# Kernel tuning notes

Measured on AMD Instinct MI355X. Metric: run time of the kernel, lower is better.

## Reference

```python
import math
import jax, jax.numpy as jnp
import numpy as np

N, T, D, H = 256, 128, 1024, 1024


def setup_inputs() -> dict:
    key = jax.random.key(0)
    k1, k2, k3, k4, k5 = jax.random.split(key, 5)
    x = jax.random.normal(k1, (N, T, D), dtype=jnp.float32)
    A = jax.random.normal(k2, (N, H, 4, 4), dtype=jnp.float32)
    Wx = jax.random.normal(k3, (D, 4 * H), dtype=jnp.float32) / math.sqrt(D)
    Wh = jax.random.normal(k4, (H, 4 * H), dtype=jnp.float32) / math.sqrt(H)
    Wattn = jax.random.normal(k5, (H, 4 * H), dtype=jnp.float32) / math.sqrt(H)
    b = jnp.zeros((4 * H,), dtype=jnp.float32)
    return {"x": x, "A": A, "Wx": Wx, "Wh": Wh, "Wattn": Wattn, "b": b}


def reference(x, A, Wx, Wh, Wattn, b):
    n, h = A.shape[0], A.shape[1]
    Af = A.reshape(n, h, 16)           # (N, H, 16) flattened 4x4 feature map
    h0 = Af.mean(axis=2)               # mean-pooled global feature inits h0, c0
    scale = 1.0 / math.sqrt(h)

    def step(carry, x_t):
        prev_h, prev_c = carry
        # scaled dot-product attention over 16 spatial locations
        logits = jnp.einsum("nh,nhl->nl", prev_h, Af) * scale   # (N, 16)
        w = jax.nn.softmax(logits, axis=1)
        attn = jnp.einsum("nhl,nl->nh", Af, w)                  # (N, H)
        # LSTM gates
        pre = x_t @ Wx + prev_h @ Wh + attn @ Wattn + b          # (N, 4H)
        i, f, o, g = jnp.split(pre, 4, axis=1)
        next_c = jax.nn.sigmoid(f) * prev_c + jax.nn.sigmoid(i) * jnp.tanh(g)
        next_h = jax.nn.sigmoid(o) * jnp.tanh(next_c)
        return (next_h, next_c), next_h

    xs = jnp.swapaxes(x, 0, 1)         # (T, N, D)
    _, hs = jax.lax.scan(step, (h0, h0), xs)
    return jnp.swapaxes(hs, 0, 1)      # (N, T, H)
```

## Files before the change

kernel.cpp:

```cpp
#include <hip/hip_runtime.h>
#include <hip/hip_bf16.h>

#define NB 256
#define TT 128
#define DD 1024
#define HH 1024
#define FH 4096
#define KTOT 3072

typedef __attribute__((ext_vector_type(4))) float f32x4;
typedef __attribute__((ext_vector_type(8))) short short8;

__device__ __forceinline__ unsigned short f2bf(float f) {
    union { float f; unsigned u; } v; v.f = f;
    unsigned u = v.u;
    u += 0x7FFFu + ((u >> 16) & 1u);
    return (unsigned short)(u >> 16);
}
__device__ __forceinline__ float bf2f(unsigned short u) {
    union { unsigned u; float f; } v; v.u = ((unsigned)u) << 16; return v.f;
}
__device__ __forceinline__ float sigm(float v) { return 1.f / (1.f + __expf(-v)); }
__device__ __forceinline__ float tanhf_(float v) { return 1.f - 2.f / (__expf(2.f * v) + 1.f); }

__device__ __forceinline__ void bmap(int bid, int& m0, int& j0) {
    int xx = bid & 7, yy = (bid >> 3) & 7, mt = bid >> 6;
    m0 = mt * 64;
    j0 = (xx * 8 + yy) * 16;
}

__device__ __forceinline__ short8 pack8(float4 v0, float4 v1) {
    short8 r;
    r[0] = (short)f2bf(v0.x); r[1] = (short)f2bf(v0.y);
    r[2] = (short)f2bf(v0.z); r[3] = (short)f2bf(v0.w);
    r[4] = (short)f2bf(v1.x); r[5] = (short)f2bf(v1.y);
    r[6] = (short)f2bf(v1.z); r[7] = (short)f2bf(v1.w);
    return r;
}

__global__ __launch_bounds__(256) void wt_prep(const float* __restrict__ Wx,
                                               const float* __restrict__ Wh,
                                               const float* __restrict__ Wattn,
                                               unsigned short* __restrict__ Wt) {
    __shared__ unsigned short tile[64][65];
    int k0 = blockIdx.x * 64;
    int c0 = blockIdx.y * 64;
    const float* src; int kl0;
    if (k0 < 1024)      { src = Wx;    kl0 = k0; }
    else if (k0 < 2048) { src = Wh;    kl0 = k0 - 1024; }
    else                { src = Wattn; kl0 = k0 - 2048; }
    int tid = threadIdx.x;
    int r = tid >> 2;
    int ch = (tid & 3) << 4;
    const float* p = src + (size_t)(kl0 + r) * FH + c0 + ch;
#pragma unroll
    for (int i = 0; i < 16; i += 4) {
        float4 v = *reinterpret_cast<const float4*>(p + i);
        tile[r][ch + i + 0] = f2bf(v.x);
        tile[r][ch + i + 1] = f2bf(v.y);
        tile[r][ch + i + 2] = f2bf(v.z);
        tile[r][ch + i + 3] = f2bf(v.w);
    }
    __syncthreads();
    alignas(16) unsigned short vals[16];
#pragma unroll
    for (int i = 0; i < 16; ++i) vals[i] = tile[ch + i][r];
    unsigned short* q = Wt + (size_t)(c0 + r) * KTOT + k0 + ch;
    *reinterpret_cast<uint4*>(q)     = *reinterpret_cast<uint4*>(&vals[0]);
    *reinterpret_cast<uint4*>(q + 8) = *reinterpret_cast<uint4*>(&vals[8]);
}

__global__ __launch_bounds__(256) void zero_buf(float* __restrict__ p, int n) {
    int i = blockIdx.x * 256 + threadIdx.x;
    if (i < n) p[i] = 0.f;
}

__global__ __launch_bounds__(256) void xconv(const float* __restrict__ x,
                                             unsigned short* __restrict__ xbf) {
    size_t i = ((size_t)blockIdx.x * 256 + threadIdx.x) * 8;
    float4 v0 = *reinterpret_cast<const float4*>(x + i);
    float4 v1 = *reinterpret_cast<const float4*>(x + i + 4);
    short8 p = pack8(v0, v1);
    *reinterpret_cast<short8*>(xbf + i) = p;
}

__global__ __launch_bounds__(256) void afT_prep(const float* __restrict__ A,
                                                unsigned short* __restrict__ AfT) {
    int n = blockIdx.x;
#pragma unroll
    for (int pass = 0; pass < 4; ++pass) {
        int hh = pass * 256 + threadIdx.x;
        const float4* p = reinterpret_cast<const float4*>(A + ((size_t)n * HH + hh) * 16);
        float4 a0 = p[0], a1 = p[1], a2 = p[2], a3 = p[3];
        float av[16] = {a0.x,a0.y,a0.z,a0.w, a1.x,a1.y,a1.z,a1.w,
                        a2.x,a2.y,a2.z,a2.w, a3.x,a3.y,a3.z,a3.w};
#pragma unroll
        for (int l = 0; l < 16; ++l)
            AfT[((size_t)n * 16 + l) * HH + hh] = f2bf(av[l]);
    }
}

__global__ __launch_bounds__(256) void g_gemm(const unsigned short* __restrict__ AfT,
                                              const unsigned short* __restrict__ Wt,
                                              unsigned short* __restrict__ G) {
    int mt = blockIdx.y;
    int ct = blockIdx.x;
    int tid = threadIdx.x;
    int w = tid >> 6, lane = tid & 63;
    int wm = w >> 1, wn = w & 1;
    int cw = lane & 15, k8 = (lane >> 4) << 3;

    const unsigned short* ap[4];
    const unsigned short* bp[4];
#pragma unroll
    for (int mf = 0; mf < 4; ++mf)
        ap[mf] = AfT + (size_t)(mt * 128 + wm * 64 + mf * 16 + cw) * HH + k8;
#pragma unroll
    for (int fn = 0; fn < 4; ++fn)
        bp[fn] = Wt + (size_t)(ct * 128 + wn * 64 + fn * 16 + cw) * KTOT + 2048 + k8;

    f32x4 acc[4][4];
#pragma unroll
    for (int mf = 0; mf < 4; ++mf)
#pragma unroll
        for (int fn = 0; fn < 4; ++fn)
#pragma unroll
            for (int e = 0; e < 4; ++e) acc[mf][fn][e] = 0.f;

#pragma unroll 4
    for (int ch = 0; ch < 32; ++ch) {
        short8 a[4], b[4];
#pragma unroll
        for (int i = 0; i < 4; ++i)
            a[i] = *reinterpret_cast<const short8*>(ap[i] + ch * 32);
#pragma unroll
        for (int i = 0; i < 4; ++i)
            b[i] = *reinterpret_cast<const short8*>(bp[i] + ch * 32);
#pragma unroll
        for (int mf = 0; mf < 4; ++mf)
#pragma unroll
            for (int fn = 0; fn < 4; ++fn)
                acc[mf][fn] = __builtin_amdgcn_mfma_f32_16x16x32_bf16(
                    a[mf], b[fn], acc[mf][fn], 0, 0, 0);
    }

    int l0 = (lane >> 4) << 2;
#pragma unroll
    for (int mf = 0; mf < 4; ++mf) {
        int n = mt * 8 + wm * 4 + mf;
#pragma unroll
        for (int fn = 0; fn < 4; ++fn) {
            int cc = ct * 128 + wn * 64 + fn * 16 + cw;
            unsigned lo = (unsigned)f2bf(acc[mf][fn][0]) | ((unsigned)f2bf(acc[mf][fn][1]) << 16);
            unsigned hi = (unsigned)f2bf(acc[mf][fn][2]) | ((unsigned)f2bf(acc[mf][fn][3]) << 16);
            uint2 val; val.x = lo; val.y = hi;
            *reinterpret_cast<uint2*>(G + ((size_t)n * FH + cc) * 16 + l0) = val;
        }
    }
}

__global__ __launch_bounds__(512) void init_kernel(const float* __restrict__ A,
                                                   float* __restrict__ c,
                                                   unsigned short* __restrict__ h0,
                                                   float* __restrict__ lg0) {
    int m0, j0; bmap(blockIdx.x, m0, j0);
    int tid = threadIdx.x;
    int r = tid >> 3, j2 = (tid & 7) * 2;
    int n = m0 + r;
    float lg[16];
#pragma unroll
    for (int l = 0; l < 16; ++l) lg[l] = 0.f;
#pragma unroll
    for (int e = 0; e < 2; ++e) {
        int j = j0 + j2 + e;
        const float4* p = reinterpret_cast<const float4*>(A + ((size_t)n * HH + j) * 16);
        float4 a0 = p[0], a1 = p[1], a2 = p[2], a3 = p[3];
        float av[16] = {a0.x,a0.y,a0.z,a0.w, a1.x,a1.y,a1.z,a1.w,
                        a2.x,a2.y,a2.z,a2.w, a3.x,a3.y,a3.z,a3.w};
        float s = 0.f;
#pragma unroll
        for (int l = 0; l < 16; ++l) s += av[l];
        float m = s * 0.0625f;
        c[(size_t)n * HH + j] = m;
        h0[(size_t)n * HH + j] = f2bf(m);
#pragma unroll
        for (int l = 0; l < 16; ++l) lg[l] += m * av[l];
    }
#pragma unroll
    for (int l = 0; l < 16; ++l) {
        lg[l] += __shfl_xor(lg[l], 1);
        lg[l] += __shfl_xor(lg[l], 2);
        lg[l] += __shfl_xor(lg[l], 4);
    }
    int l0 = (tid & 7) * 2;
    atomicAdd(&lg0[(size_t)n * 16 + l0],     lg[l0]);
    atomicAdd(&lg0[(size_t)n * 16 + l0 + 1], lg[l0 + 1]);
}

template<bool XBF>
__global__ __launch_bounds__(1024)
void gemm_step(const float* __restrict__ x, const unsigned short* __restrict__ xbf,
               const unsigned short* __restrict__ hprev, unsigned short* __restrict__ hnext,
               const unsigned short* __restrict__ Wt, const unsigned short* __restrict__ G,
               const float* __restrict__ A, const float* __restrict__ bb,
               const float* __restrict__ lgcur, float* __restrict__ lgnext,
               float* __restrict__ lgz, float* __restrict__ c,
               float* __restrict__ out, int t) {
    __shared__ float red[2][64][68];
    int m0, j0; bmap(blockIdx.x, m0, j0);
    int tid = threadIdx.x;
    int w = tid >> 6, lane = tid & 63;
    int wk = w & 3, wn = (w >> 2) & 1, wm = w >> 3;
    int cw = lane & 15, k8 = (lane >> 4) << 3;

    f32x4 acc[2][2];
#pragma unroll
    for (int mf = 0; mf < 2; ++mf)
#pragma unroll
        for (int fn = 0; fn < 2; ++fn)
#pragma unroll
            for (int e = 0; e < 4; ++e) acc[mf][fn][e] = 0.f;

    const unsigned short* bp[2];
    int kbase = (wk < 2) ? wk * 512 : 1024 + (wk - 2) * 512;
#pragma unroll
    for (int fn = 0; fn < 2; ++fn) {
        int col = wn * 32 + fn * 16 + cw;
        int brow = (col >> 4) * 1024 + j0 + (col & 15);
        bp[fn] = Wt + (size_t)brow * KTOT + kbase + k8;
    }

    if (wk < 2) {
        if (XBF) {
            const unsigned short* ap[2];
#pragma unroll
            for (int mf = 0; mf < 2; ++mf)
                ap[mf] = xbf + ((size_t)(m0 + wm * 32 + mf * 16 + cw) * TT + t) * DD
                             + wk * 512 + k8;
#pragma unroll 4
            for (int ch = 0; ch < 16; ++ch) {
                short8 a0 = *reinterpret_cast<const short8*>(ap[0] + ch * 32);
                short8 a1 = *reinterpret_cast<const short8*>(ap[1] + ch * 32);
                short8 b0 = *reinterpret_cast<const short8*>(bp[0] + ch * 32);
                short8 b1 = *reinterpret_cast<const short8*>(bp[1] + ch * 32);
                acc[0][0] = __builtin_amdgcn_mfma_f32_16x16x32_bf16(a0, b0, acc[0][0], 0, 0, 0);
                acc[0][1] = __builtin_amdgcn_mfma_f32_16x16x32_bf16(a0, b1, acc[0][1], 0, 0, 0);
                acc[1][0] = __builtin_amdgcn_mfma_f32_16x16x32_bf16(a1, b0, acc[1][0], 0, 0, 0);
                acc[1][1] = __builtin_amdgcn_mfma_f32_16x16x32_bf16(a1, b1, acc[1][1], 0, 0, 0);
            }
        } else {
            const float* ap[2];
#pragma unroll
            for (int mf = 0; mf < 2; ++mf)
                ap[mf] = x + ((size_t)(m0 + wm * 32 + mf * 16 + cw) * TT + t) * DD
                           + wk * 512 + k8;
#pragma unroll 2
            for (int ch = 0; ch < 16; ++ch) {
                float4 u0 = *reinterpret_cast<const float4*>(ap[0] + ch * 32);
                float4 u1 = *reinterpret_cast<const float4*>(ap[0] + ch * 32 + 4);
                float4 v0 = *reinterpret_cast<const float4*>(ap[1] + ch * 32);
                float4 v1 = *reinterpret_cast<const float4*>(ap[1] + ch * 32 + 4);
                short8 a0 = pack8(u0, u1);
                short8 a1 = pack8(v0, v1);
                short8 b0 = *reinterpret_cast<const short8*>(bp[0] + ch * 32);
                short8 b1 = *reinterpret_cast<const short8*>(bp[1] + ch * 32);
                acc[0][0] = __builtin_amdgcn_mfma_f32_16x16x32_bf16(a0, b0, acc[0][0], 0, 0, 0);
                acc[0][1] = __builtin_amdgcn_mfma_f32_16x16x32_bf16(a0, b1, acc[0][1], 0, 0, 0);
                acc[1][0] = __builtin_amdgcn_mfma_f32_16x16x32_bf16(a1, b0, acc[1][0], 0, 0, 0);
                acc[1][1] = __builtin_amdgcn_mfma_f32_16x16x32_bf16(a1, b1, acc[1][1], 0, 0, 0);
            }
        }
    } else {
        const unsigned short* ap[2];
#pragma unroll
        for (int mf = 0; mf < 2; ++mf)
            ap[mf] = hprev + (size_t)(m0 + wm * 32 + mf * 16 + cw) * HH
                          + (wk - 2) * 512 + k8;
#pragma unroll 4
        for (int ch = 0; ch < 16; ++ch) {
            short8 a0 = *reinterpret_cast<const short8*>(ap[0] + ch * 32);
            short8 a1 = *reinterpret_cast<const short8*>(ap[1] + ch * 32);
            short8 b0 = *reinterpret_cast<const short8*>(bp[0] + ch * 32);
            short8 b1 = *reinterpret_cast<const short8*>(bp[1] + ch * 32);
            acc[0][0] = __builtin_amdgcn_mfma_f32_16x16x32_bf16(a0, b0, acc[0][0], 0, 0, 0);
            acc[0][1] = __builtin_amdgcn_mfma_f32_16x16x32_bf16(a0, b1, acc[0][1], 0, 0, 0);
            acc[1][0] = __builtin_amdgcn_mfma_f32_16x16x32_bf16(a1, b0, acc[1][0], 0, 0, 0);
            acc[1][1] = __builtin_amdgcn_mfma_f32_16x16x32_bf16(a1, b1, acc[1][1], 0, 0, 0);
        }
    }

    int r0 = (lane >> 4) << 2;
    if (wk < 2) {
#pragma unroll
        for (int mf = 0; mf < 2; ++mf)
#pragma unroll
            for (int fn = 0; fn < 2; ++fn)
                *reinterpret_cast<f32x4*>(
                    &red[wk][wn * 32 + fn * 16 + cw][wm * 32 + mf * 16 + r0]) = acc[mf][fn];
    }
    __syncthreads();
    if (wk >= 2) {
#pragma unroll
        for (int mf = 0; mf < 2; ++mf)
#pragma unroll
            for (int fn = 0; fn < 2; ++fn) {
                float* p = &red[wk - 2][wn * 32 + fn * 16 + cw][wm * 32 + mf * 16 + r0];
                f32x4 v = *reinterpret_cast<const f32x4*>(p);
                v += acc[mf][fn];
                *reinterpret_cast<f32x4*>(p) = v;
            }
    }
    __syncthreads();

    int r = tid >> 4, j1 = tid & 15;
    int n = m0 + r;
    int j = j0 + j1;

    float sm[16];
    {
        const float4* lp = reinterpret_cast<const float4*>(lgcur + (size_t)n * 16);
        float4 s0 = lp[0], s1 = lp[1], s2 = lp[2], s3 = lp[3];
        float s[16] = {s0.x,s0.y,s0.z,s0.w, s1.x,s1.y,s1.z,s1.w,
                       s2.x,s2.y,s2.z,s2.w, s3.x,s3.y,s3.z,s3.w};
        float mx = -1e30f;
#pragma unroll
        for (int l = 0; l < 16; ++l) { s[l] *= 0.03125f; mx = fmaxf(mx, s[l]); }
        float sum = 0.f;
#pragma unroll
        for (int l = 0; l < 16; ++l) { sm[l] = __expf(s[l] - mx); sum += sm[l]; }
        float inv = 1.f / sum;
#pragma unroll
        for (int l = 0; l < 16; ++l) sm[l] *= inv;
    }

    float pre[4];
#pragma unroll
    for (int g = 0; g < 4; ++g) {
        int colL = g * 16 + j1;
        float p = red[0][colL][r] + red[1][colL][r] + bb[g * HH + j];
        const unsigned short* gp = G + ((size_t)n * FH + g * HH + j) * 16;
        uint4 g0 = *reinterpret_cast<const uint4*>(gp);
        uint4 g1 = *reinterpret_cast<const uint4*>(gp + 8);
        const unsigned* gu = reinterpret_cast<const unsigned*>(&g0);
        const unsigned* gv = reinterpret_cast<const unsigned*>(&g1);
        float d = 0.f;
#pragma unroll
        for (int q = 0; q < 4; ++q) {
            d += sm[q * 2]     * bf2f((unsigned short)(gu[q] & 0xFFFF));
            d += sm[q * 2 + 1] * bf2f((unsigned short)(gu[q] >> 16));
        }
#pragma unroll
        for (int q = 0; q < 4; ++q) {
            d += sm[8 + q * 2]     * bf2f((unsigned short)(gv[q] & 0xFFFF));
            d += sm[8 + q * 2 + 1] * bf2f((unsigned short)(gv[q] >> 16));
        }
        pre[g] = p + d;
    }

    float cv = c[(size_t)n * HH + j];
    float ig = sigm(pre[0]);
    float fg = sigm(pre[1]);
    float og = sigm(pre[2]);
    float gg = tanhf_(pre[3]);
    float cn = fg * cv + ig * gg;
    float hn = og * tanhf_(cn);
    c[(size_t)n * HH + j] = cn;
    hnext[(size_t)n * HH + j] = f2bf(hn);
    out[((size_t)n * TT + t) * HH + j] = hn;

    if ((blockIdx.x & 63) == 0)
        lgz[(size_t)n * 16 + j1] = 0.f;

    float lg[16];
    {
        const float4* p = reinterpret_cast<const float4*>(A + ((size_t)n * HH + j) * 16);
        float4 a0 = p[0], a1 = p[1], a2 = p[2], a3 = p[3];
        lg[0]=hn*a0.x;  lg[1]=hn*a0.y;  lg[2]=hn*a0.z;  lg[3]=hn*a0.w;
        lg[4]=hn*a1.x;  lg[5]=hn*a1.y;  lg[6]=hn*a1.z;  lg[7]=hn*a1.w;
        lg[8]=hn*a2.x;  lg[9]=hn*a2.y;  lg[10]=hn*a2.z; lg[11]=hn*a2.w;
        lg[12]=hn*a3.x; lg[13]=hn*a3.y; lg[14]=hn*a3.z; lg[15]=hn*a3.w;
    }
#pragma unroll
    for (int l = 0; l < 16; ++l) {
        lg[l] += __shfl_xor(lg[l], 1);
        lg[l] += __shfl_xor(lg[l], 2);
        lg[l] += __shfl_xor(lg[l], 4);
        lg[l] += __shfl_xor(lg[l], 8);
    }
    atomicAdd(&lgnext[(size_t)n * 16 + j1], lg[j1]);
}

extern "C" void kernel_launch(void* const* d_in, const int* in_sizes, int n_in,
                              void* d_out, int out_size, void* d_ws, size_t ws_size,
                              hipStream_t stream) {
    const float* x     = (const float*)d_in[0];
    const float* A     = (const float*)d_in[1];
    const float* Wx    = (const float*)d_in[2];
    const float* Wh    = (const float*)d_in[3];
    const float* Wattn = (const float*)d_in[4];
    const float* b     = (const float*)d_in[5];
    float* out = (float*)d_out;

    char* ws = (char*)d_ws;
    unsigned short* Wt   = (unsigned short*)(ws);
    unsigned short* G    = (unsigned short*)(ws + 25165824);
    unsigned short* AfT  = (unsigned short*)(ws + 58720256);
    unsigned short* hbuf = (unsigned short*)(ws + 67108864);
    float* c             = (float*)(ws + 68157440);
    float* lg            = (float*)(ws + 69206016);
    unsigned short* xbf  = (unsigned short*)(ws + 69255168);
    bool use_xbf = ws_size >= (size_t)69255168 + 67108864;

    wt_prep<<<dim3(48, 64), 256, 0, stream>>>(Wx, Wh, Wattn, Wt);
    zero_buf<<<48, 256, 0, stream>>>(lg, 3 * NB * 16);
    afT_prep<<<NB, 256, 0, stream>>>(A, AfT);
    g_gemm<<<dim3(32, 32), 256, 0, stream>>>(AfT, Wt, G);
    init_kernel<<<256, 512, 0, stream>>>(A, c, hbuf, lg);
    if (use_xbf) xconv<<<16384, 256, 0, stream>>>(x, xbf);

    for (int t = 0; t < TT; ++t) {
        const unsigned short* hp = hbuf + (size_t)(t & 1) * NB * HH;
        unsigned short* hx       = hbuf + (size_t)((t & 1) ^ 1) * NB * HH;
        float* lgc  = lg + (size_t)(t % 3) * NB * 16;
        float* lgn  = lg + (size_t)((t + 1) % 3) * NB * 16;
        float* lgzz = lg + (size_t)((t + 2) % 3) * NB * 16;
        if (use_xbf)
            gemm_step<true><<<256, 1024, 0, stream>>>(x, xbf, hp, hx, Wt, G, A, b,
                                                      lgc, lgn, lgzz, c, out, t);
        else
            gemm_step<false><<<256, 1024, 0, stream>>>(x, xbf, hp, hx, Wt, G, A, b,
                                                       lgc, lgn, lgzz, c, out, t);
    }
}
```

Baseline: 5.164 ms.

## Fuse per-timestep launches into one persistent cooperative kernel with grid sync

Replaces the 128 per-timestep gemm_step launches with a single cooperative kernel that loops over time and uses grid.sync between steps, removing per-launch overhead and inter-kernel gaps. The next-step attention logits now read the precomputed bf16 AfT layout with h staged in shared memory, replacing fp32 A loads plus cross-lane shuffles. Bias is hoisted out of the loop, and G and out use nontemporal accesses. Costs include a grid-wide barrier each step, reliance on all 256 blocks of 1024 threads being co-resident, and bf16 rounding of A in the logit path.

```diff
diff --git a/kernel.cpp b/kernel.cpp
--- a/kernel.cpp
+++ b/kernel.cpp
@@ -1,5 +1,8 @@
 #include <hip/hip_runtime.h>
 #include <hip/hip_bf16.h>
+#include <hip/hip_cooperative_groups.h>
+
+namespace cg = cooperative_groups;
 
 #define NB 256
 #define TT 128
@@ -10,6 +13,7 @@
 
 typedef __attribute__((ext_vector_type(4))) float f32x4;
 typedef __attribute__((ext_vector_type(8))) short short8;
+typedef __attribute__((ext_vector_type(4))) unsigned u32x4;
 
 __device__ __forceinline__ unsigned short f2bf(float f) {
     union { float f; unsigned u; } v; v.f = f;
@@ -199,195 +203,212 @@
 
 template<bool XBF>
 __global__ __launch_bounds__(1024)
-void gemm_step(const float* __restrict__ x, const unsigned short* __restrict__ xbf,
-               const unsigned short* __restrict__ hprev, unsigned short* __restrict__ hnext,
-               const unsigned short* __restrict__ Wt, const unsigned short* __restrict__ G,
-               const float* __restrict__ A, const float* __restrict__ bb,
-               const float* __restrict__ lgcur, float* __restrict__ lgnext,
-               float* __restrict__ lgz, float* __restrict__ c,
-               float* __restrict__ out, int t) {
+void lstm_persist(const float* __restrict__ x, const unsigned short* __restrict__ xbf,
+                  unsigned short* __restrict__ hbuf,
+                  const unsigned short* __restrict__ Wt,
+                  const unsigned short* __restrict__ G,
+                  const unsigned short* __restrict__ AfT,
+                  const float* __restrict__ bb,
+                  float* __restrict__ lg,
+                  float* __restrict__ c,
+                  float* __restrict__ out) {
+    cg::grid_group grid = cg::this_grid();
     __shared__ float red[2][64][68];
+    __shared__ float hn_s[64][16];
+
     int m0, j0; bmap(blockIdx.x, m0, j0);
-    int tid = threadIdx.x;
-    int w = tid >> 6, lane = tid & 63;
-    int wk = w & 3, wn = (w >> 2) & 1, wm = w >> 3;
-    int cw = lane & 15, k8 = (lane >> 4) << 3;
-
-    f32x4 acc[2][2];
-#pragma unroll
-    for (int mf = 0; mf < 2; ++mf)
-#pragma unroll
-        for (int fn = 0; fn < 2; ++fn)
-#pragma unroll
-            for (int e = 0; e < 4; ++e) acc[mf][fn][e] = 0.f;
-
-    const unsigned short* bp[2];
-    int kbase = (wk < 2) ? wk * 512 : 1024 + (wk - 2) * 512;
-#pragma unroll
-    for (int fn = 0; fn < 2; ++fn) {
-        int col = wn * 32 + fn * 16 + cw;
-        int brow = (col >> 4) * 1024 + j0 + (col & 15);
-        bp[fn] = Wt + (size_t)brow * KTOT + kbase + k8;
-    }
-
-    if (wk < 2) {
-        if (XBF) {
-            const unsigned short* ap[2];
-#pragma unroll
-            for (int mf = 0; mf < 2; ++mf)
-                ap[mf] = xbf + ((size_t)(m0 + wm * 32 + mf * 16 + cw) * TT + t) * DD
-                             + wk * 512 + k8;
+    const int tid = threadIdx.x;
+    const int w = tid >> 6, lane = tid & 63;
+    const int wk = w & 3, wn = (w >> 2) & 1, wm = w >> 3;
+    const int cw = lane & 15, k8 = (lane >> 4) << 3;
+
+    const unsigned short* bp0;
+    const unsigned short* bp1;
+    {
+        const int kbase = (wk < 2) ? wk * 512 : 1024 + (wk - 2) * 512;
+        int col0 = wn * 32 + cw;
+        int col1 = wn * 32 + 16 + cw;
+        bp0 = Wt + (size_t)((col0 >> 4) * 1024 + j0 + (col0 & 15)) * KTOT + kbase + k8;
+        bp1 = Wt + (size_t)((col1 >> 4) * 1024 + j0 + (col1 & 15)) * KTOT + kbase + k8;
+    }
+    const int arow0 = m0 + wm * 32 + cw;
+    const int arow1 = arow0 + 16;
+    const size_t xoff0 = (size_t)arow0 * TT * DD + (size_t)wk * 512 + k8;
+    const size_t xoff1 = (size_t)arow1 * TT * DD + (size_t)wk * 512 + k8;
+    const size_t hoff0 = (size_t)arow0 * HH + (size_t)(wk - 2) * 512 + k8;
+    const size_t hoff1 = (size_t)arow1 * HH + (size_t)(wk - 2) * 512 + k8;
+
+    const int er = tid >> 4, ej = tid & 15;
+    const int en = m0 + er;
+    const int ejj = j0 + ej;
+    const bool zeroer = ((blockIdx.x & 63) == 0);
+    const float bias[4] = { bb[0 * HH + ejj], bb[1 * HH + ejj],
+                            bb[2 * HH + ejj], bb[3 * HH + ejj] };
+    const unsigned short* afp = AfT + ((size_t)en * 16 + ej) * HH + j0;
+
+    for (int t = 0; t < TT; ++t) {
+        const unsigned short* hprev = hbuf + (size_t)(t & 1) * (NB * HH);
+        unsigned short* hnext       = hbuf + (size_t)((t & 1) ^ 1) * (NB * HH);
+        const float* lgcur = lg + (size_t)(t % 3) * (NB * 16);
+        float* lgnext      = lg + (size_t)((t + 1) % 3) * (NB * 16);
+        float* lgz         = lg + (size_t)((t + 2) % 3) * (NB * 16);
+
+        f32x4 acc[2][2];
+#pragma unroll
+        for (int mf = 0; mf < 2; ++mf)
+#pragma unroll
+            for (int fn = 0; fn < 2; ++fn)
+#pragma unroll
+                for (int e = 0; e < 4; ++e) acc[mf][fn][e] = 0.f;
+
+        if (wk < 2) {
+            if (XBF) {
+                const unsigned short* a0p = xbf + xoff0 + (size_t)t * DD;
+                const unsigned short* a1p = xbf + xoff1 + (size_t)t * DD;
+#pragma unroll 4
+                for (int ch = 0; ch < 16; ++ch) {
+                    short8 a0 = *reinterpret_cast<const short8*>(a0p + ch * 32);
+                    short8 a1 = *reinterpret_cast<const short8*>(a1p + ch * 32);
+                    short8 b0 = *reinterpret_cast<const short8*>(bp0 + ch * 32);
+                    short8 b1 = *reinterpret_cast<const short8*>(bp1 + ch * 32);
+                    acc[0][0] = __builtin_amdgcn_mfma_f32_16x16x32_bf16(a0, b0, acc[0][0], 0, 0, 0);
+                    acc[0][1] = __builtin_amdgcn_mfma_f32_16x16x32_bf16(a0, b1, acc[0][1], 0, 0, 0);
+                    acc[1][0] = __builtin_amdgcn_mfma_f32_16x16x32_bf16(a1, b0, acc[1][0], 0, 0, 0);
+                    acc[1][1] = __builtin_amdgcn_mfma_f32_16x16x32_bf16(a1, b1, acc[1][1], 0, 0, 0);
+                }
+            } else {
+                const float* a0p = x + xoff0 + (size_t)t * DD;
+                const float* a1p = x + xoff1 + (size_t)t * DD;
+#pragma unroll 2
+                for (int ch = 0; ch < 16; ++ch) {
+                    float4 u0 = *reinterpret_cast<const float4*>(a0p + ch * 32);
+                    float4 u1 = *reinterpret_cast<const float4*>(a0p + ch * 32 + 4);
+                    float4 v0 = *reinterpret_cast<const float4*>(a1p + ch * 32);
+                    float4 v1 = *reinterpret_cast<const float4*>(a1p + ch * 32 + 4);
+                    short8 a0 = pack8(u0, u1);
+                    short8 a1 = pack8(v0, v1);
+                    short8 b0 = *reinterpret_cast<const short8*>(bp0 + ch * 32);
+                    short8 b1 = *reinterpret_cast<const short8*>(bp1 + ch * 32);
+                    acc[0][0] = __builtin_amdgcn_mfma_f32_16x16x32_bf16(a0, b0, acc[0][0], 0, 0, 0);
+                    acc[0][1] = __builtin_amdgcn_mfma_f32_16x16x32_bf16(a0, b1, acc[0][1], 0, 0, 0);
+                    acc[1][0] = __builtin_amdgcn_mfma_f32_16x16x32_bf16(a1, b0, acc[1][0], 0, 0, 0);
+                    acc[1][1] = __builtin_amdgcn_mfma_f32_16x16x32_bf16(a1, b1, acc[1][1], 0, 0, 0);
+                }
+            }
+        } else {
+            const unsigned short* a0p = hprev + hoff0;
+            const unsigned short* a1p = hprev + hoff1;
 #pragma unroll 4
             for (int ch = 0; ch < 16; ++ch) {
-                short8 a0 = *reinterpret_cast<const short8*>(ap[0] + ch * 32);
-                short8 a1 = *reinterpret_cast<const short8*>(ap[1] + ch * 32);
-                short8 b0 = *reinterpret_cast<const short8*>(bp[0] + ch * 32);
-                short8 b1 = *reinterpret_cast<const short8*>(bp[1] + ch * 32);
+                short8 a0 = *reinterpret_cast<const short8*>(a0p + ch * 32);
+                short8 a1 = *reinterpret_cast<const short8*>(a1p + ch * 32);
+                short8 b0 = *reinterpret_cast<const short8*>(bp0 + ch * 32);
+                short8 b1 = *reinterpret_cast<const short8*>(bp1 + ch * 32);
                 acc[0][0] = __builtin_amdgcn_mfma_f32_16x16x32_bf16(a0, b0, acc[0][0], 0, 0, 0);
                 acc[0][1] = __builtin_amdgcn_mfma_f32_16x16x32_bf16(a0, b1, acc[0][1], 0, 0, 0);
                 acc[1][0] = __builtin_amdgcn_mfma_f32_16x16x32_bf16(a1, b0, acc[1][0], 0, 0, 0);
                 acc[1][1] = __builtin_amdgcn_mfma_f32_16x16x32_bf16(a1, b1, acc[1][1], 0, 0, 0);
             }
-        } else {
-            const float* ap[2];
+        }
+
+        int r0 = (lane >> 4) << 2;
+        if (wk < 2) {
 #pragma unroll
             for (int mf = 0; mf < 2; ++mf)
-                ap[mf] = x + ((size_t)(m0 + wm * 32 + mf * 16 + cw) * TT + t) * DD
-                           + wk * 512 + k8;
-#pragma unroll 2
-            for (int ch = 0; ch < 16; ++ch) {
-                float4 u0 = *reinterpret_cast<const float4*>(ap[0] + ch * 32);
-                float4 u1 = *reinterpret_cast<const float4*>(ap[0] + ch * 32 + 4);
-                float4 v0 = *reinterpret_cast<const float4*>(ap[1] + ch * 32);
-                float4 v1 = *reinterpret_cast<const float4*>(ap[1] + ch * 32 + 4);
-                short8 a0 = pack8(u0, u1);
-                short8 a1 = pack8(v0, v1);
-                short8 b0 = *reinterpret_cast<const short8*>(bp[0] + ch * 32);
-                short8 b1 = *reinterpret_cast<const short8*>(bp[1] + ch * 32);
-                acc[0][0] = __builtin_amdgcn_mfma_f32_16x16x32_bf16(a0, b0, acc[0][0], 0, 0, 0);
-                acc[0][1] = __builtin_amdgcn_mfma_f32_16x16x32_bf16(a0, b1, acc[0][1], 0, 0, 0);
-                acc[1][0] = __builtin_amdgcn_mfma_f32_16x16x32_bf16(a1, b0, acc[1][0], 0, 0, 0);
-                acc[1][1] = __builtin_amdgcn_mfma_f32_16x16x32_bf16(a1, b1, acc[1][1], 0, 0, 0);
-            }
-        }
-    } else {
-        const unsigned short* ap[2];
-#pragma unroll
-        for (int mf = 0; mf < 2; ++mf)
-            ap[mf] = hprev + (size_t)(m0 + wm * 32 + mf * 16 + cw) * HH
-                          + (wk - 2) * 512 + k8;
-#pragma unroll 4
-        for (int ch = 0; ch < 16; ++ch) {
-            short8 a0 = *reinterpret_cast<const short8*>(ap[0] + ch * 32);
-            short8 a1 = *reinterpret_cast<const short8*>(ap[1] + ch * 32);
-            short8 b0 = *reinterpret_cast<const short8*>(bp[0] + ch * 32);
-            short8 b1 = *reinterpret_cast<const short8*>(bp[1] + ch * 32);
-            acc[0][0] = __builtin_amdgcn_mfma_f32_16x16x32_bf16(a0, b0, acc[0][0], 0, 0, 0);
-            acc[0][1] = __builtin_amdgcn_mfma_f32_16x16x32_bf16(a0, b1, acc[0][1], 0, 0, 0);
-            acc[1][0] = __builtin_amdgcn_mfma_f32_16x16x32_bf16(a1, b0, acc[1][0], 0, 0, 0);
-            acc[1][1] = __builtin_amdgcn_mfma_f32_16x16x32_bf16(a1, b1, acc[1][1], 0, 0, 0);
-        }
-    }
-
-    int r0 = (lane >> 4) << 2;
-    if (wk < 2) {
-#pragma unroll
-        for (int mf = 0; mf < 2; ++mf)
-#pragma unroll
-            for (int fn = 0; fn < 2; ++fn)
-                *reinterpret_cast<f32x4*>(
-                    &red[wk][wn * 32 + fn * 16 + cw][wm * 32 + mf * 16 + r0]) = acc[mf][fn];
-    }
-    __syncthreads();
-    if (wk >= 2) {
-#pragma unroll
-        for (int mf = 0; mf < 2; ++mf)
-#pragma unroll
-            for (int fn = 0; fn < 2; ++fn) {
-                float* p = &red[wk - 2][wn * 32 + fn * 16 + cw][wm * 32 + mf * 16 + r0];
-                f32x4 v = *reinterpret_cast<const f32x4*>(p);
-                v += acc[mf][fn];
-                *reinterpret_cast<f32x4*>(p) = v;
-            }
-    }
-    __syncthreads();
-
-    int r = tid >> 4, j1 = tid & 15;
-    int n = m0 + r;
-    int j = j0 + j1;
-
-    float sm[16];
-    {
-        const float4* lp = reinterpret_cast<const float4*>(lgcur + (size_t)n * 16);
-        float4 s0 = lp[0], s1 = lp[1], s2 = lp[2], s3 = lp[3];
-        float s[16] = {s0.x,s0.y,s0.z,s0.w, s1.x,s1.y,s1.z,s1.w,
-                       s2.x,s2.y,s2.z,s2.w, s3.x,s3.y,s3.z,s3.w};
-        float mx = -1e30f;
-#pragma unroll
-        for (int l = 0; l < 16; ++l) { s[l] *= 0.03125f; mx = fmaxf(mx, s[l]); }
-        float sum = 0.f;
-#pragma unroll
-        for (int l = 0; l < 16; ++l) { sm[l] = __expf(s[l] - mx); sum += sm[l]; }
-        float inv = 1.f / sum;
-#pragma unroll
-        for (int l = 0; l < 16; ++l) sm[l] *= inv;
-    }
-
-    float pre[4];
-#pragma unroll
-    for (int g = 0; g < 4; ++g) {
-        int colL = g * 16 + j1;
-        float p = red[0][colL][r] + red[1][colL][r] + bb[g * HH + j];
-        const unsigned short* gp = G + ((size_t)n * FH + g * HH + j) * 16;
-        uint4 g0 = *reinterpret_cast<const uint4*>(gp);
-        uint4 g1 = *reinterpret_cast<const uint4*>(gp + 8);
-        const unsigned* gu = reinterpret_cast<const unsigned*>(&g0);
-        const unsigned* gv = reinterpret_cast<const unsigned*>(&g1);
-        float d = 0.f;
-#pragma unroll
-        for (int q = 0; q < 4; ++q) {
-            d += sm[q * 2]     * bf2f((unsigned short)(gu[q] & 0xFFFF));
-            d += sm[q * 2 + 1] * bf2f((unsigned short)(gu[q] >> 16));
-        }
-#pragma unroll
-        for (int q = 0; q < 4; ++q) {
-            d += sm[8 + q * 2]     * bf2f((unsigned short)(gv[q] & 0xFFFF));
-            d += sm[8 + q * 2 + 1] * bf2f((unsigned short)(gv[q] >> 16));
-        }
-        pre[g] = p + d;
-    }
-
-    float cv = c[(size_t)n * HH + j];
-    float ig = sigm(pre[0]);
-    float fg = sigm(pre[1]);
-    float og = sigm(pre[2]);
-    float gg = tanhf_(pre[3]);
-    float cn = fg * cv + ig * gg;
-    float hn = og * tanhf_(cn);
-    c[(size_t)n * HH + j] = cn;
-    hnext[(size_t)n * HH + j] = f2bf(hn);
-    out[((size_t)n * TT + t) * HH + j] = hn;
-
-    if ((blockIdx.x & 63) == 0)
-        lgz[(size_t)n * 16 + j1] = 0.f;
-
-    float lg[16];
-    {
-        const float4* p = reinterpret_cast<const float4*>(A + ((size_t)n * HH + j) * 16);
-        float4 a0 = p[0], a1 = p[1], a2 = p[2], a3 = p[3];
-        lg[0]=hn*a0.x;  lg[1]=hn*a0.y;  lg[2]=hn*a0.z;  lg[3]=hn*a0.w;
-        lg[4]=hn*a1.x;  lg[5]=hn*a1.y;  lg[6]=hn*a1.z;  lg[7]=hn*a1.w;
-        lg[8]=hn*a2.x;  lg[9]=hn*a2.y;  lg[10]=hn*a2.z; lg[11]=hn*a2.w;
-        lg[12]=hn*a3.x; lg[13]=hn*a3.y; lg[14]=hn*a3.z; lg[15]=hn*a3.w;
-    }
-#pragma unroll
-    for (int l = 0; l < 16; ++l) {
-        lg[l] += __shfl_xor(lg[l], 1);
-        lg[l] += __shfl_xor(lg[l], 2);
-        lg[l] += __shfl_xor(lg[l], 4);
-        lg[l] += __shfl_xor(lg[l], 8);
-    }
-    atomicAdd(&lgnext[(size_t)n * 16 + j1], lg[j1]);
+#pragma unroll
+                for (int fn = 0; fn < 2; ++fn)
+                    *reinterpret_cast<f32x4*>(
+                        &red[wk][wn * 32 + fn * 16 + cw][wm * 32 + mf * 16 + r0]) = acc[mf][fn];
+        }
+        __syncthreads();
+        if (wk >= 2) {
+#pragma unroll
+            for (int mf = 0; mf < 2; ++mf)
+#pragma unroll
+                for (int fn = 0; fn < 2; ++fn) {
+                    float* p = &red[wk - 2][wn * 32 + fn * 16 + cw][wm * 32 + mf * 16 + r0];
+                    f32x4 v = *reinterpret_cast<const f32x4*>(p);
+                    v += acc[mf][fn];
+                    *reinterpret_cast<f32x4*>(p) = v;
+                }
+        }
+        __syncthreads();
+
+        float sm[16];
+        {
+            const float4* lp = reinterpret_cast<const float4*>(lgcur + (size_t)en * 16);
+            float4 s0 = lp[0], s1 = lp[1], s2 = lp[2], s3 = lp[3];
+            float s[16] = {s0.x,s0.y,s0.z,s0.w, s1.x,s1.y,s1.z,s1.w,
+                           s2.x,s2.y,s2.z,s2.w, s3.x,s3.y,s3.z,s3.w};
+            float mx = -1e30f;
+#pragma unroll
+            for (int l = 0; l < 16; ++l) { s[l] *= 0.03125f; mx = fmaxf(mx, s[l]); }
+            float sum = 0.f;
+#pragma unroll
+            for (int l = 0; l < 16; ++l) { sm[l] = __expf(s[l] - mx); sum += sm[l]; }
+            float inv = 1.f / sum;
+#pragma unroll
+            for (int l = 0; l < 16; ++l) sm[l] *= inv;
+        }
+
+        float pre[4];
+#pragma unroll
+        for (int g = 0; g < 4; ++g) {
+            int colL = g * 16 + ej;
+            float p = red[0][colL][er] + red[1][colL][er] + bias[g];
+            const u32x4* gp = reinterpret_cast<const u32x4*>(
+                G + ((size_t)en * FH + g * HH + ejj) * 16);
+            u32x4 g0 = __builtin_nontemporal_load(gp);
+            u32x4 g1 = __builtin_nontemporal_load(gp + 1);
+            float d = 0.f;
+#pragma unroll
+            for (int q = 0; q < 4; ++q) {
+                d += sm[q * 2]     * bf2f((unsigned short)(g0[q] & 0xFFFF));
+                d += sm[q * 2 + 1] * bf2f((unsigned short)(g0[q] >> 16));
+            }
+#pragma unroll
+            for (int q = 0; q < 4; ++q) {
+                d += sm[8 + q * 2]     * bf2f((unsigned short)(g1[q] & 0xFFFF));
+                d += sm[8 + q * 2 + 1] * bf2f((unsigned short)(g1[q] >> 16));
+            }
+            pre[g] = p + d;
+        }
+
+        float cv = c[(size_t)en * HH + ejj];
+        float ig = sigm(pre[0]);
+        float fg = sigm(pre[1]);
+        float og = sigm(pre[2]);
+        float gg = tanhf_(pre[3]);
+        float cn = fg * cv + ig * gg;
+        float hn = og * tanhf_(cn);
+        c[(size_t)en * HH + ejj] = cn;
+        hnext[(size_t)en * HH + ejj] = f2bf(hn);
+        __builtin_nontemporal_store(hn, out + ((size_t)en * TT + t) * HH + ejj);
+        hn_s[er][ej] = hn;
+        if (zeroer) lgz[(size_t)en * 16 + ej] = 0.f;
+        __syncthreads();
+
+        {
+            uint4 q0 = *reinterpret_cast<const uint4*>(afp);
+            uint4 q1 = *reinterpret_cast<const uint4*>(afp + 8);
+            const unsigned* au = reinterpret_cast<const unsigned*>(&q0);
+            const unsigned* av = reinterpret_cast<const unsigned*>(&q1);
+            float part = 0.f;
+#pragma unroll
+            for (int q = 0; q < 4; ++q) {
+                part += hn_s[er][q * 2]     * bf2f((unsigned short)(au[q] & 0xFFFF));
+                part += hn_s[er][q * 2 + 1] * bf2f((unsigned short)(au[q] >> 16));
+            }
+#pragma unroll
+            for (int q = 0; q < 4; ++q) {
+                part += hn_s[er][8 + q * 2]     * bf2f((unsigned short)(av[q] & 0xFFFF));
+                part += hn_s[er][8 + q * 2 + 1] * bf2f((unsigned short)(av[q] >> 16));
+            }
+            atomicAdd(&lgnext[(size_t)en * 16 + ej], part);
+        }
+
+        grid.sync();
+    }
 }
 
 extern "C" void kernel_launch(void* const* d_in, const int* in_sizes, int n_in,
@@ -398,7 +419,7 @@
     const float* Wx    = (const float*)d_in[2];
     const float* Wh    = (const float*)d_in[3];
     const float* Wattn = (const float*)d_in[4];
-    const float* b     = (const float*)d_in[5];
+    const float* bptr  = (const float*)d_in[5];
     float* out = (float*)d_out;
 
     char* ws = (char*)d_ws;
@@ -418,17 +439,9 @@
     init_kernel<<<256, 512, 0, stream>>>(A, c, hbuf, lg);
     if (use_xbf) xconv<<<16384, 256, 0, stream>>>(x, xbf);
 
-    for (int t = 0; t < TT; ++t) {
-        const unsigned short* hp = hbuf + (size_t)(t & 1) * NB * HH;
-        unsigned short* hx       = hbuf + (size_t)((t & 1) ^ 1) * NB * HH;
-        float* lgc  = lg + (size_t)(t % 3) * NB * 16;
-        float* lgn  = lg + (size_t)((t + 1) % 3) * NB * 16;
-        float* lgzz = lg + (size_t)((t + 2) % 3) * NB * 16;
-        if (use_xbf)
-            gemm_step<true><<<256, 1024, 0, stream>>>(x, xbf, hp, hx, Wt, G, A, b,
-                                                      lgc, lgn, lgzz, c, out, t);
-        else
-            gemm_step<false><<<256, 1024, 0, stream>>>(x, xbf, hp, hx, Wt, G, A, b,
-                                                       lgc, lgn, lgzz, c, out, t);
-    }
-}
+    void* args[] = { (void*)&x, (void*)&xbf, (void*)&hbuf, (void*)&Wt, (void*)&G,
+                     (void*)&AfT, (void*)&bptr, (void*)&lg, (void*)&c, (void*)&out };
+    const void* kfn = use_xbf ? reinterpret_cast<const void*>(&lstm_persist<true>)
+                              : reinterpret_cast<const void*>(&lstm_persist<false>);
+    (void)hipLaunchCooperativeKernel(kfn, dim3(256), dim3(1024), args, 0, stream);
+}
```

After: 8.305 ms. 1.61x slower.
